# Kernel tuning notes

Measured on AMD Instinct MI355X. Metric: run time of the kernel, lower is better.

## Reference

```python
import jax, jax.numpy as jnp
import numpy as np

EMBED_DIM = 512
N_HEADS = 8
HEAD_DIM = EMBED_DIM // N_HEADS


def setup_inputs() -> dict:
    key = jax.random.key(0)
    ks = jax.random.split(key, 8)
    B, S, D = 8, 2048, EMBED_DIM
    scale = 1.0 / np.sqrt(D)
    return {
        "key": jax.random.normal(ks[0], (B, S, D), dtype=jnp.float32),
        "query": jax.random.normal(ks[1], (B, S, D), dtype=jnp.float32),
        "value": jax.random.normal(ks[2], (B, S, D), dtype=jnp.float32),
        # nn.Linear stores weight as [out, in]; y = x @ W.T. We store W_T=[in,out].
        "Wq": jax.random.normal(ks[3], (D, D), dtype=jnp.float32) * scale,
        "Wk": jax.random.normal(ks[4], (D, D), dtype=jnp.float32) * scale,
        "Wv": jax.random.normal(ks[5], (D, D), dtype=jnp.float32) * scale,
        "Wo": jax.random.normal(ks[6], (D, D), dtype=jnp.float32) * scale,
        "bo": jax.random.normal(ks[7], (D,), dtype=jnp.float32) * scale,
    }


def reference(key, query, value, Wq, Wk, Wv, Wo, bo):
    B, S, D = key.shape
    Sq = query.shape[1]
    H, Hd = N_HEADS, HEAD_DIM
    # projections (no bias for q/k/v)
    q = (query @ Wq).reshape(B, Sq, H, Hd)
    k = (key @ Wk).reshape(B, S, H, Hd)
    v = (value @ Wv).reshape(B, S, H, Hd)
    # scores: [B, H, Sq, S]
    product = jnp.einsum("bqhd,bkhd->bhqk", q, k) / np.sqrt(Hd)
    scores = jax.nn.softmax(product, axis=-1)
    out = jnp.einsum("bhqk,bkhd->bqhd", scores, v).reshape(B, Sq, D)
    return out @ Wo + bo
```

## Files before the change

### kernel.cpp

```cpp
#include <hip/hip_runtime.h>

typedef _Float16 half8 __attribute__((ext_vector_type(8)));
typedef _Float16 half4 __attribute__((ext_vector_type(4)));
typedef __fp16 fp16x2 __attribute__((ext_vector_type(2)));
typedef float floatx16 __attribute__((ext_vector_type(16)));
typedef unsigned int uint2v __attribute__((ext_vector_type(2)));

#define MFMA_F16 __builtin_amdgcn_mfma_f32_32x32x16_f16

__device__ __forceinline__ float fast_exp2(float x) {
#if __has_builtin(__builtin_amdgcn_exp2f)
    return __builtin_amdgcn_exp2f(x);
#else
    return exp2f(x);
#endif
}

__device__ __forceinline__ half4 pack4(float a, float b, float c, float d) {
    union { fp16x2 p[2]; half4 h; } u;
    u.p[0] = __builtin_amdgcn_cvt_pkrtz(a, b);
    u.p[1] = __builtin_amdgcn_cvt_pkrtz(c, d);
    return u.h;
}

__device__ __forceinline__ unsigned int pk2(float a, float b) {
    union { fp16x2 p; unsigned int u; } v;
    v.p = __builtin_amdgcn_cvt_pkrtz(a, b);
    return v.u;
}

__device__ __forceinline__ half8 ld_frag_lds(const _Float16* p) {
    union { half8 v; half4 h[2]; } u;
    u.h[0] = *(const half4*)(p);
    u.h[1] = *(const half4*)(p + 4);
    return u.v;
}

__device__ __forceinline__ half8 pv_frag(const unsigned int* w, int i0) {
    uint2v s0 = __builtin_amdgcn_permlane32_swap(w[2 * i0 + 0], w[2 * i0 + 2], false, false);
    uint2v s1 = __builtin_amdgcn_permlane32_swap(w[2 * i0 + 1], w[2 * i0 + 3], false, false);
    union { unsigned int u[4]; half8 h; } pu;
    pu.u[0] = s0[0];
    pu.u[1] = s1[0];
    pu.u[2] = s0[1];
    pu.u[3] = s1[1];
    return pu.h;
}

__global__ __launch_bounds__(256) void wcvt_kernel(const float* __restrict__ Wq,
                                                   const float* __restrict__ Wk,
                                                   const float* __restrict__ Wv,
                                                   const float* __restrict__ Wo,
                                                   _Float16* __restrict__ Wt) {
    __shared__ _Float16 T[64 * 68];
    const int bx   = blockIdx.x;
    const int wsel = bx >> 6;
    const int tile = bx & 63;
    const int to   = (tile >> 3) * 64;
    const int ti   = (tile & 7) * 64;
    const float* src = (wsel == 0) ? Wq : (wsel == 1) ? Wk : (wsel == 2) ? Wv : Wo;
    const int t = threadIdx.x;
    const int rloc = t >> 4, c4 = (t & 15) * 4;
#pragma unroll
    for (int m = 0; m < 4; m++) {
        int i = ti + rloc + 16 * m;
        float4 f = *(const float4*)(src + (size_t)i * 512 + to + c4);
        T[(c4 + 0) * 68 + rloc + 16 * m] = (_Float16)f.x;
        T[(c4 + 1) * 68 + rloc + 16 * m] = (_Float16)f.y;
        T[(c4 + 2) * 68 + rloc + 16 * m] = (_Float16)f.z;
        T[(c4 + 3) * 68 + rloc + 16 * m] = (_Float16)f.w;
    }
    __syncthreads();
    const int o_loc = t >> 2, ich = (t & 3) * 16;
    const _Float16* s = &T[o_loc * 68 + ich];
    _Float16* dst = Wt + (size_t)wsel * 262144 + (size_t)(to + o_loc) * 512 + ti + ich;
    half4 a0 = *(const half4*)(s);
    half4 a1 = *(const half4*)(s + 4);
    half4 a2 = *(const half4*)(s + 8);
    half4 a3 = *(const half4*)(s + 12);
    *(half4*)(dst)      = a0;
    *(half4*)(dst + 4)  = a1;
    *(half4*)(dst + 8)  = a2;
    *(half4*)(dst + 12) = a3;
}

__global__ __launch_bounds__(256, 3) void qkv_gemm(const float* __restrict__ query,
                                                   const float* __restrict__ key,
                                                   const float* __restrict__ value,
                                                   const _Float16* __restrict__ Wt,
                                                   _Float16* __restrict__ Qh,
                                                   _Float16* __restrict__ Kh,
                                                   _Float16* __restrict__ Vt,
                                                   float C1) {
    __shared__ _Float16 Alds[128 * 68];
    __shared__ _Float16 Blds[128 * 68];

    const int z = blockIdx.z;
    const float* A = (z == 0) ? query : (z == 1) ? key : value;
    const _Float16* W = Wt + (size_t)z * 262144;

    const int tid  = threadIdx.x;
    const int lane = tid & 63;
    const int w    = tid >> 6;
    const int l31  = lane & 31;
    const int lh   = lane >> 5;
    const int wm   = w >> 1;
    const int wn   = w & 1;
    const int n0   = blockIdx.x * 128;
    const int m0   = blockIdx.y * 128;
    const int crow = tid >> 3;
    const int ck8  = (tid & 7) * 8;

    floatx16 acc[2][2];
#pragma unroll
    for (int i = 0; i < 2; i++)
#pragma unroll
        for (int j = 0; j < 2; j++)
#pragma unroll
            for (int r = 0; r < 16; r++) acc[i][j][r] = 0.0f;

    float4 apre[4][2];
    int4   bpre[4];
#pragma unroll
    for (int i = 0; i < 4; i++) {
        const float* p = A + (size_t)(m0 + crow + 32 * i) * 512 + ck8;
        apre[i][0] = *(const float4*)(p);
        apre[i][1] = *(const float4*)(p + 4);
        bpre[i] = *(const int4*)(W + (size_t)(n0 + crow + 32 * i) * 512 + ck8);
    }

    for (int t = 0; t < 8; t++) {
        __syncthreads();
#pragma unroll
        for (int i = 0; i < 4; i++) {
            int r = crow + 32 * i;
            float4 f0 = apre[i][0], f1 = apre[i][1];
            *(half4*)&Alds[r * 68 + ck8]     = pack4(f0.x, f0.y, f0.z, f0.w);
            *(half4*)&Alds[r * 68 + ck8 + 4] = pack4(f1.x, f1.y, f1.z, f1.w);
            *(int2*)&Blds[r * 68 + ck8]      = make_int2(bpre[i].x, bpre[i].y);
            *(int2*)&Blds[r * 68 + ck8 + 4]  = make_int2(bpre[i].z, bpre[i].w);
        }
        __syncthreads();
        if (t < 7) {
            int ks2 = (t + 1) * 64;
#pragma unroll
            for (int i = 0; i < 4; i++) {
                const float* p = A + (size_t)(m0 + crow + 32 * i) * 512 + ks2 + ck8;
                apre[i][0] = *(const float4*)(p);
                apre[i][1] = *(const float4*)(p + 4);
                bpre[i] = *(const int4*)(W + (size_t)(n0 + crow + 32 * i) * 512 + ks2 + ck8);
            }
        }
#pragma unroll
        for (int kc = 0; kc < 4; kc++) {
            int kb = kc * 16 + lh * 8;
            half8 af[2], bf[2];
            af[0] = ld_frag_lds(&Alds[(wm * 64 + l31) * 68 + kb]);
            af[1] = ld_frag_lds(&Alds[(wm * 64 + 32 + l31) * 68 + kb]);
            bf[0] = ld_frag_lds(&Blds[(wn * 64 + l31) * 68 + kb]);
            bf[1] = ld_frag_lds(&Blds[(wn * 64 + 32 + l31) * 68 + kb]);
#pragma unroll
            for (int i = 0; i < 2; i++)
#pragma unroll
                for (int j = 0; j < 2; j++)
                    acc[i][j] = MFMA_F16(af[i], bf[j], acc[i][j], 0, 0, 0);
        }
    }

    const float oscale = (z == 0) ? C1 : 1.0f;
    _Float16* out01 = (z == 0) ? Qh : Kh;
#pragma unroll
    for (int i = 0; i < 2; i++) {
#pragma unroll
        for (int j = 0; j < 2; j++) {
            int gn    = n0 + wn * 64 + j * 32 + l31;
            int mbase = m0 + wm * 64 + i * 32 + 4 * lh;
            int h = gn >> 6, hd = gn & 63;
            if (z < 2) {
#pragma unroll
                for (int r = 0; r < 16; r++) {
                    int gm = mbase + (r & 3) + 8 * (r >> 2);
                    int b = gm >> 11, s = gm & 2047;
                    out01[(size_t)((b * 8 + h) * 2048 + s) * 64 + hd] =
                        (_Float16)(acc[i][j][r] * oscale);
                }
            } else {
#pragma unroll
                for (int g = 0; g < 4; g++) {
                    int gm = mbase + 8 * g;
                    int b = gm >> 11, s = gm & 2047;
                    *(half4*)&Vt[(size_t)((b * 8 + h) * 64 + hd) * 2048 + s] =
                        pack4(acc[i][j][4 * g + 0], acc[i][j][4 * g + 1],
                              acc[i][j][4 * g + 2], acc[i][j][4 * g + 3]);
                }
            }
        }
    }
}

__global__ __launch_bounds__(256, 3) void out_gemm(const _Float16* __restrict__ A,
                                                   const _Float16* __restrict__ W,
                                                   const float* __restrict__ bias,
                                                   float* __restrict__ out) {
    __shared__ _Float16 Alds[128 * 68];
    __shared__ _Float16 Blds[128 * 68];

    const int tid  = threadIdx.x;
    const int lane = tid & 63;
    const int w    = tid >> 6;
    const int l31  = lane & 31;
    const int lh   = lane >> 5;
    const int wm   = w >> 1;
    const int wn   = w & 1;
    const int n0   = blockIdx.x * 128;
    const int m0   = blockIdx.y * 128;
    const int crow = tid >> 3;
    const int ck8  = (tid & 7) * 8;

    floatx16 acc[2][2];
#pragma unroll
    for (int i = 0; i < 2; i++)
#pragma unroll
        for (int j = 0; j < 2; j++)
#pragma unroll
            for (int r = 0; r < 16; r++) acc[i][j][r] = 0.0f;

    int4 apre[4], bpre[4];
#pragma unroll
    for (int i = 0; i < 4; i++) {
        apre[i] = *(const int4*)(A + (size_t)(m0 + crow + 32 * i) * 512 + ck8);
        bpre[i] = *(const int4*)(W + (size_t)(n0 + crow + 32 * i) * 512 + ck8);
    }

    for (int t = 0; t < 8; t++) {
        __syncthreads();
#pragma unroll
        for (int i = 0; i < 4; i++) {
            int r = crow + 32 * i;
            *(int2*)&Alds[r * 68 + ck8]     = make_int2(apre[i].x, apre[i].y);
            *(int2*)&Alds[r * 68 + ck8 + 4] = make_int2(apre[i].z, apre[i].w);
            *(int2*)&Blds[r * 68 + ck8]     = make_int2(bpre[i].x, bpre[i].y);
            *(int2*)&Blds[r * 68 + ck8 + 4] = make_int2(bpre[i].z, bpre[i].w);
        }
        __syncthreads();
        if (t < 7) {
            int ks2 = (t + 1) * 64;
#pragma unroll
            for (int i = 0; i < 4; i++) {
                apre[i] = *(const int4*)(A + (size_t)(m0 + crow + 32 * i) * 512 + ks2 + ck8);
                bpre[i] = *(const int4*)(W + (size_t)(n0 + crow + 32 * i) * 512 + ks2 + ck8);
            }
        }
#pragma unroll
        for (int kc = 0; kc < 4; kc++) {
            int kb = kc * 16 + lh * 8;
            half8 af[2], bf[2];
            af[0] = ld_frag_lds(&Alds[(wm * 64 + l31) * 68 + kb]);
            af[1] = ld_frag_lds(&Alds[(wm * 64 + 32 + l31) * 68 + kb]);
            bf[0] = ld_frag_lds(&Blds[(wn * 64 + l31) * 68 + kb]);
            bf[1] = ld_frag_lds(&Blds[(wn * 64 + 32 + l31) * 68 + kb]);
#pragma unroll
            for (int i = 0; i < 2; i++)
#pragma unroll
                for (int j = 0; j < 2; j++)
                    acc[i][j] = MFMA_F16(af[i], bf[j], acc[i][j], 0, 0, 0);
        }
    }

#pragma unroll
    for (int i = 0; i < 2; i++) {
#pragma unroll
        for (int j = 0; j < 2; j++) {
            int gn    = n0 + wn * 64 + j * 32 + l31;
            int mbase = m0 + wm * 64 + i * 32 + 4 * lh;
            float bv = bias[gn];
#pragma unroll
            for (int r = 0; r < 16; r++) {
                int gm = mbase + (r & 3) + 8 * (r >> 2);
                out[(size_t)gm * 512 + gn] = acc[i][j][r] + bv;
            }
        }
    }
}

__global__ __launch_bounds__(256, 3) void attn_kernel(const _Float16* __restrict__ Qg,
                                                      const _Float16* __restrict__ Kg,
                                                      const _Float16* __restrict__ Vg,
                                                      _Float16* __restrict__ AO) {
    __shared__ _Float16 Kbuf[2][64 * 68];
    __shared__ _Float16 Vbuf[2][64 * 68];

    const int tid  = threadIdx.x;
    const int lane = tid & 63;
    const int w    = tid >> 6;
    const int l31  = lane & 31;
    const int lh   = lane >> 5;
    const int h    = blockIdx.y;
    const int b    = blockIdx.z;
    const int q0   = blockIdx.x * 128 + w * 32;

    const size_t bhoff = (size_t)(b * 8 + h) * (2048 * 64);
    const _Float16* Qbh = Qg + bhoff;
    const _Float16* Kbh = Kg + bhoff;
    const _Float16* Vbh = Vg + bhoff;

    const int c0row = tid >> 3, ck8 = (tid & 7) * 8;
    const int c1row = c0row + 32;

    half8 qf[4];
#pragma unroll
    for (int kc = 0; kc < 4; kc++)
        qf[kc] = *(const half8*)(Qbh + (size_t)(q0 + l31) * 64 + kc * 16 + lh * 8);

    floatx16 O[2];
#pragma unroll
    for (int i = 0; i < 2; i++)
#pragma unroll
        for (int r = 0; r < 16; r++) O[i][r] = 0.0f;
    float lsum = 0.0f;

    unsigned int w16[16];
    half8 vf[4][2];

    int4 kpre[2], vpre[2];
    kpre[0] = *(const int4*)(Kbh + c0row * 64 + ck8);
    kpre[1] = *(const int4*)(Kbh + c1row * 64 + ck8);
    vpre[0] = *(const int4*)(Vbh + (size_t)c0row * 2048 + ck8);
    vpre[1] = *(const int4*)(Vbh + (size_t)c1row * 2048 + ck8);
    *(int2*)&Kbuf[0][c0row * 68 + ck8]     = make_int2(kpre[0].x, kpre[0].y);
    *(int2*)&Kbuf[0][c0row * 68 + ck8 + 4] = make_int2(kpre[0].z, kpre[0].w);
    *(int2*)&Kbuf[0][c1row * 68 + ck8]     = make_int2(kpre[1].x, kpre[1].y);
    *(int2*)&Kbuf[0][c1row * 68 + ck8 + 4] = make_int2(kpre[1].z, kpre[1].w);
    *(int2*)&Vbuf[0][c0row * 68 + ck8]     = make_int2(vpre[0].x, vpre[0].y);
    *(int2*)&Vbuf[0][c0row * 68 + ck8 + 4] = make_int2(vpre[0].z, vpre[0].w);
    *(int2*)&Vbuf[0][c1row * 68 + ck8]     = make_int2(vpre[1].x, vpre[1].y);
    *(int2*)&Vbuf[0][c1row * 68 + ck8 + 4] = make_int2(vpre[1].z, vpre[1].w);
    kpre[0] = *(const int4*)(Kbh + 4096 + c0row * 64 + ck8);
    kpre[1] = *(const int4*)(Kbh + 4096 + c1row * 64 + ck8);
    vpre[0] = *(const int4*)(Vbh + 64 + (size_t)c0row * 2048 + ck8);
    vpre[1] = *(const int4*)(Vbh + 64 + (size_t)c1row * 2048 + ck8);
    __syncthreads();

    for (int kt = 0; kt < 32; kt++) {
        const int cur = kt & 1;
        const _Float16* Kc = Kbuf[cur];
        const _Float16* Vc = Vbuf[cur];

        if (kt > 0) {
#pragma unroll
            for (int kc = 0; kc < 4; kc++) {
                int i0 = (kc >> 1) * 4 + (kc & 1) * 2;
                half8 pf = pv_frag(w16, i0);
                O[0] = MFMA_F16(vf[kc][0], pf, O[0], 0, 0, 0);
                O[1] = MFMA_F16(vf[kc][1], pf, O[1], 0, 0, 0);
            }
        }

        if (kt < 31) {
            _Float16* Kd = Kbuf[cur ^ 1];
            _Float16* Vd = Vbuf[cur ^ 1];
            *(int2*)&Kd[c0row * 68 + ck8]     = make_int2(kpre[0].x, kpre[0].y);
            *(int2*)&Kd[c0row * 68 + ck8 + 4] = make_int2(kpre[0].z, kpre[0].w);
            *(int2*)&Kd[c1row * 68 + ck8]     = make_int2(kpre[1].x, kpre[1].y);
            *(int2*)&Kd[c1row * 68 + ck8 + 4] = make_int2(kpre[1].z, kpre[1].w);
            *(int2*)&Vd[c0row * 68 + ck8]     = make_int2(vpre[0].x, vpre[0].y);
            *(int2*)&Vd[c0row * 68 + ck8 + 4] = make_int2(vpre[0].z, vpre[0].w);
            *(int2*)&Vd[c1row * 68 + ck8]     = make_int2(vpre[1].x, vpre[1].y);
            *(int2*)&Vd[c1row * 68 + ck8 + 4] = make_int2(vpre[1].z, vpre[1].w);
        }
        if (kt < 30) {
            const _Float16* Ksrc = Kbh + (size_t)(kt + 2) * 4096;
            const _Float16* Vsrc = Vbh + (size_t)(kt + 2) * 64;
            kpre[0] = *(const int4*)(Ksrc + c0row * 64 + ck8);
            kpre[1] = *(const int4*)(Ksrc + c1row * 64 + ck8);
            vpre[0] = *(const int4*)(Vsrc + (size_t)c0row * 2048 + ck8);
            vpre[1] = *(const int4*)(Vsrc + (size_t)c1row * 2048 + ck8);
        }

#pragma unroll
        for (int kc = 0; kc < 4; kc++) {
            vf[kc][0] = ld_frag_lds(&Vc[(l31)*68      + kc * 16 + lh * 8]);
            vf[kc][1] = ld_frag_lds(&Vc[(32 + l31)*68 + kc * 16 + lh * 8]);
        }

        floatx16 Sf[2];
#pragma unroll
        for (int i = 0; i < 2; i++)
#pragma unroll
            for (int r = 0; r < 16; r++) Sf[i][r] = 0.0f;
#pragma unroll
        for (int kc = 0; kc < 4; kc++) {
#pragma unroll
            for (int ms = 0; ms < 2; ms++) {
                half8 kf = ld_frag_lds(&Kc[(ms * 32 + l31) * 68 + kc * 16 + lh * 8]);
                Sf[ms] = MFMA_F16(kf, qf[kc], Sf[ms], 0, 0, 0);
            }
        }

        float rsA = 0.0f, rsB = 0.0f;
#pragma unroll
        for (int i = 0; i < 8; i++) {
            int ms = i >> 2, g = i & 3;
            float p0 = fast_exp2(Sf[ms][4 * g + 0]);
            float p1 = fast_exp2(Sf[ms][4 * g + 1]);
            float p2 = fast_exp2(Sf[ms][4 * g + 2]);
            float p3 = fast_exp2(Sf[ms][4 * g + 3]);
            rsA += p0 + p1;
            rsB += p2 + p3;
            w16[2 * i + 0] = pk2(p0, p1);
            w16[2 * i + 1] = pk2(p2, p3);
        }
        lsum += rsA + rsB;

        __syncthreads();
    }

#pragma unroll
    for (int kc = 0; kc < 4; kc++) {
        int i0 = (kc >> 1) * 4 + (kc & 1) * 2;
        half8 pf = pv_frag(w16, i0);
        O[0] = MFMA_F16(vf[kc][0], pf, O[0], 0, 0, 0);
        O[1] = MFMA_F16(vf[kc][1], pf, O[1], 0, 0, 0);
    }

    lsum += __shfl_xor(lsum, 32);
    float inv = 1.0f / lsum;
    int q = q0 + l31;
#pragma unroll
    for (int hs = 0; hs < 2; hs++) {
#pragma unroll
        for (int g = 0; g < 4; g++) {
            *(half4*)&AO[(size_t)(b * 2048 + q) * 512 + h * 64 + hs * 32 + g * 8 + lh * 4] =
                pack4(O[hs][4 * g + 0] * inv, O[hs][4 * g + 1] * inv,
                      O[hs][4 * g + 2] * inv, O[hs][4 * g + 3] * inv);
        }
    }
}

extern "C" void kernel_launch(void* const* d_in, const int* in_sizes, int n_in,
                              void* d_out, int out_size, void* d_ws, size_t ws_size,
                              hipStream_t stream) {
    const float* key   = (const float*)d_in[0];
    const float* query = (const float*)d_in[1];
    const float* value = (const float*)d_in[2];
    const float* Wq    = (const float*)d_in[3];
    const float* Wk    = (const float*)d_in[4];
    const float* Wv    = (const float*)d_in[5];
    const float* Wo    = (const float*)d_in[6];
    const float* bo    = (const float*)d_in[7];

    _Float16* ws = (_Float16*)d_ws;
    _Float16* Wt = ws;
    _Float16* Qh = ws + 1048576;
    _Float16* Kh = Qh + 8388608;
    _Float16* Vt = Kh + 8388608;
    _Float16* AO = Vt + 8388608;

    const float C1 = 0.18033688011112042f;

    wcvt_kernel<<<dim3(256), dim3(256), 0, stream>>>(Wq, Wk, Wv, Wo, Wt);

    qkv_gemm<<<dim3(4, 128, 3), dim3(256), 0, stream>>>(query, key, value, Wt,
                                                        Qh, Kh, Vt, C1);

    attn_kernel<<<dim3(16, 8, 8), dim3(256), 0, stream>>>(Qh, Kh, Vt, AO);

    out_gemm<<<dim3(4, 128), dim3(256), 0, stream>>>(AO, Wt + 3 * 262144, bo,
                                                     (float*)d_out);
}
```

Measured before the change: 290.2 us.

## Process 64 query rows per wave in attention to reuse K/V tiles

```diff
diff --git a/kernel.cpp b/kernel.cpp
--- a/kernel.cpp
+++ b/kernel.cpp
@@ -283,7 +283,7 @@
     }
 }
 
-__global__ __launch_bounds__(256, 3) void attn_kernel(const _Float16* __restrict__ Qg,
+__global__ __launch_bounds__(256, 2) void attn_kernel(const _Float16* __restrict__ Qg,
                                                       const _Float16* __restrict__ Kg,
                                                       const _Float16* __restrict__ Vg,
                                                       _Float16* __restrict__ AO) {
@@ -297,7 +297,7 @@
     const int lh   = lane >> 5;
     const int h    = blockIdx.y;
     const int b    = blockIdx.z;
-    const int q0   = blockIdx.x * 128 + w * 32;
+    const int q0   = blockIdx.x * 256 + w * 64;
 
     const size_t bhoff = (size_t)(b * 8 + h) * (2048 * 64);
     const _Float16* Qbh = Qg + bhoff;
@@ -307,19 +307,24 @@
     const int c0row = tid >> 3, ck8 = (tid & 7) * 8;
     const int c1row = c0row + 32;
 
-    half8 qf[4];
+    half8 qf[4][2];
 #pragma unroll
     for (int kc = 0; kc < 4; kc++)
-        qf[kc] = *(const half8*)(Qbh + (size_t)(q0 + l31) * 64 + kc * 16 + lh * 8);
-
-    floatx16 O[2];
+#pragma unroll
+        for (int qs = 0; qs < 2; qs++)
+            qf[kc][qs] = *(const half8*)(Qbh + (size_t)(q0 + qs * 32 + l31) * 64 +
+                                         kc * 16 + lh * 8);
+
+    floatx16 O[2][2];
 #pragma unroll
     for (int i = 0; i < 2; i++)
 #pragma unroll
-        for (int r = 0; r < 16; r++) O[i][r] = 0.0f;
-    float lsum = 0.0f;
-
-    unsigned int w16[16];
+        for (int j = 0; j < 2; j++)
+#pragma unroll
+            for (int r = 0; r < 16; r++) O[i][j][r] = 0.0f;
+    float lsum0 = 0.0f, lsum1 = 0.0f;
+
+    unsigned int w16[2][16];
     half8 vf[4][2];
 
     int4 kpre[2], vpre[2];
@@ -347,13 +352,18 @@
         const _Float16* Vc = Vbuf[cur];
 
         if (kt > 0) {
+            __builtin_amdgcn_s_setprio(1);
 #pragma unroll
             for (int kc = 0; kc < 4; kc++) {
                 int i0 = (kc >> 1) * 4 + (kc & 1) * 2;
-                half8 pf = pv_frag(w16, i0);
-                O[0] = MFMA_F16(vf[kc][0], pf, O[0], 0, 0, 0);
-                O[1] = MFMA_F16(vf[kc][1], pf, O[1], 0, 0, 0);
-            }
+                half8 pf0 = pv_frag(w16[0], i0);
+                half8 pf1 = pv_frag(w16[1], i0);
+                O[0][0] = MFMA_F16(vf[kc][0], pf0, O[0][0], 0, 0, 0);
+                O[1][0] = MFMA_F16(vf[kc][1], pf0, O[1][0], 0, 0, 0);
+                O[0][1] = MFMA_F16(vf[kc][0], pf1, O[0][1], 0, 0, 0);
+                O[1][1] = MFMA_F16(vf[kc][1], pf1, O[1][1], 0, 0, 0);
+            }
+            __builtin_amdgcn_s_setprio(0);
         }
 
         if (kt < 31) {
@@ -383,56 +393,88 @@
             vf[kc][1] = ld_frag_lds(&Vc[(32 + l31)*68 + kc * 16 + lh * 8]);
         }
 
-        floatx16 Sf[2];
+        floatx16 Sf[2][2];
 #pragma unroll
         for (int i = 0; i < 2; i++)
 #pragma unroll
-            for (int r = 0; r < 16; r++) Sf[i][r] = 0.0f;
+            for (int j = 0; j < 2; j++)
+#pragma unroll
+                for (int r = 0; r < 16; r++) Sf[i][j][r] = 0.0f;
 #pragma unroll
         for (int kc = 0; kc < 4; kc++) {
 #pragma unroll
             for (int ms = 0; ms < 2; ms++) {
                 half8 kf = ld_frag_lds(&Kc[(ms * 32 + l31) * 68 + kc * 16 + lh * 8]);
-                Sf[ms] = MFMA_F16(kf, qf[kc], Sf[ms], 0, 0, 0);
-            }
-        }
-
-        float rsA = 0.0f, rsB = 0.0f;
-#pragma unroll
-        for (int i = 0; i < 8; i++) {
-            int ms = i >> 2, g = i & 3;
-            float p0 = fast_exp2(Sf[ms][4 * g + 0]);
-            float p1 = fast_exp2(Sf[ms][4 * g + 1]);
-            float p2 = fast_exp2(Sf[ms][4 * g + 2]);
-            float p3 = fast_exp2(Sf[ms][4 * g + 3]);
-            rsA += p0 + p1;
-            rsB += p2 + p3;
-            w16[2 * i + 0] = pk2(p0, p1);
-            w16[2 * i + 1] = pk2(p2, p3);
-        }
-        lsum += rsA + rsB;
+                Sf[ms][0] = MFMA_F16(kf, qf[kc][0], Sf[ms][0], 0, 0, 0);
+                Sf[ms][1] = MFMA_F16(kf, qf[kc][1], Sf[ms][1], 0, 0, 0);
+            }
+        }
+
+        {
+            float rsA = 0.0f, rsB = 0.0f;
+#pragma unroll
+            for (int i = 0; i < 8; i++) {
+                int ms = i >> 2, g = i & 3;
+                float p0 = fast_exp2(Sf[ms][0][4 * g + 0]);
+                float p1 = fast_exp2(Sf[ms][0][4 * g + 1]);
+                float p2 = fast_exp2(Sf[ms][0][4 * g + 2]);
+                float p3 = fast_exp2(Sf[ms][0][4 * g + 3]);
+                rsA += p0 + p1;
+                rsB += p2 + p3;
+                w16[0][2 * i + 0] = pk2(p0, p1);
+                w16[0][2 * i + 1] = pk2(p2, p3);
+            }
+            lsum0 += rsA + rsB;
+        }
+        {
+            float rsA = 0.0f, rsB = 0.0f;
+#pragma unroll
+            for (int i = 0; i < 8; i++) {
+                int ms = i >> 2, g = i & 3;
+                float p0 = fast_exp2(Sf[ms][1][4 * g + 0]);
+                float p1 = fast_exp2(Sf[ms][1][4 * g + 1]);
+                float p2 = fast_exp2(Sf[ms][1][4 * g + 2]);
+                float p3 = fast_exp2(Sf[ms][1][4 * g + 3]);
+                rsA += p0 + p1;
+                rsB += p2 + p3;
+                w16[1][2 * i + 0] = pk2(p0, p1);
+                w16[1][2 * i + 1] = pk2(p2, p3);
+            }
+            lsum1 += rsA + rsB;
+        }
 
         __syncthreads();
     }
 
+    __builtin_amdgcn_s_setprio(1);
 #pragma unroll
     for (int kc = 0; kc < 4; kc++) {
         int i0 = (kc >> 1) * 4 + (kc & 1) * 2;
-        half8 pf = pv_frag(w16, i0);
-        O[0] = MFMA_F16(vf[kc][0], pf, O[0], 0, 0, 0);
-        O[1] = MFMA_F16(vf[kc][1], pf, O[1], 0, 0, 0);
-    }
-
-    lsum += __shfl_xor(lsum, 32);
-    float inv = 1.0f / lsum;
-    int q = q0 + l31;
-#pragma unroll
-    for (int hs = 0; hs < 2; hs++) {
-#pragma unroll
-        for (int g = 0; g < 4; g++) {
-            *(half4*)&AO[(size_t)(b * 2048 + q) * 512 + h * 64 + hs * 32 + g * 8 + lh * 4] =
-                pack4(O[hs][4 * g + 0] * inv, O[hs][4 * g + 1] * inv,
-                      O[hs][4 * g + 2] * inv, O[hs][4 * g + 3] * inv);
+        half8 pf0 = pv_frag(w16[0], i0);
+        half8 pf1 = pv_frag(w16[1], i0);
+        O[0][0] = MFMA_F16(vf[kc][0], pf0, O[0][0], 0, 0, 0);
+        O[1][0] = MFMA_F16(vf[kc][1], pf0, O[1][0], 0, 0, 0);
+        O[0][1] = MFMA_F16(vf[kc][0], pf1, O[0][1], 0, 0, 0);
+        O[1][1] = MFMA_F16(vf[kc][1], pf1, O[1][1], 0, 0, 0);
+    }
+    __builtin_amdgcn_s_setprio(0);
+
+    lsum0 += __shfl_xor(lsum0, 32);
+    lsum1 += __shfl_xor(lsum1, 32);
+    float inv0 = 1.0f / lsum0;
+    float inv1 = 1.0f / lsum1;
+#pragma unroll
+    for (int qs = 0; qs < 2; qs++) {
+        float inv = (qs == 0) ? inv0 : inv1;
+        int q = q0 + qs * 32 + l31;
+#pragma unroll
+        for (int hs = 0; hs < 2; hs++) {
+#pragma unroll
+            for (int g = 0; g < 4; g++) {
+                *(half4*)&AO[(size_t)(b * 2048 + q) * 512 + h * 64 + hs * 32 + g * 8 + lh * 4] =
+                    pack4(O[hs][qs][4 * g + 0] * inv, O[hs][qs][4 * g + 1] * inv,
+                          O[hs][qs][4 * g + 2] * inv, O[hs][qs][4 * g + 3] * inv);
+            }
         }
     }
 }
@@ -463,7 +505,7 @@
     qkv_gemm<<<dim3(4, 128, 3), dim3(256), 0, stream>>>(query, key, value, Wt,
                                                         Qh, Kh, Vt, C1);
 
-    attn_kernel<<<dim3(16, 8, 8), dim3(256), 0, stream>>>(Qh, Kh, Vt, AO);
+    attn_kernel<<<dim3(8, 8, 8), dim3(256), 0, stream>>>(Qh, Kh, Vt, AO);
 
     out_gemm<<<dim3(4, 128), dim3(256), 0, stream>>>(AO, Wt + 3 * 262144, bo,
                                                      (float*)d_out);
```

Measured after the change: 379.1 us. 30.6% more time.

## Load V fragments directly from global memory, dropping V LDS staging

Applied to the files above, without the earlier changes.

```diff
diff --git a/kernel.cpp b/kernel.cpp
--- a/kernel.cpp
+++ b/kernel.cpp
@@ -34,6 +34,12 @@
     u.h[0] = *(const half4*)(p);
     u.h[1] = *(const half4*)(p + 4);
     return u.v;
+}
+
+__device__ __forceinline__ void tile_barrier() {
+    asm volatile("s_waitcnt lgkmcnt(0)" ::: "memory");
+    __builtin_amdgcn_s_barrier();
+    asm volatile("" ::: "memory");
 }
 
 __device__ __forceinline__ half8 pv_frag(const unsigned int* w, int i0) {
@@ -288,7 +294,6 @@
                                                       const _Float16* __restrict__ Vg,
                                                       _Float16* __restrict__ AO) {
     __shared__ _Float16 Kbuf[2][64 * 68];
-    __shared__ _Float16 Vbuf[2][64 * 68];
 
     const int tid  = threadIdx.x;
     const int lane = tid & 63;
@@ -304,6 +309,9 @@
     const _Float16* Kbh = Kg + bhoff;
     const _Float16* Vbh = Vg + bhoff;
 
+    const _Float16* Vrow0 = Vbh + (size_t)l31 * 2048 + lh * 8;
+    const _Float16* Vrow1 = Vbh + (size_t)(32 + l31) * 2048 + lh * 8;
+
     const int c0row = tid >> 3, ck8 = (tid & 7) * 8;
     const int c1row = c0row + 32;
 
@@ -320,107 +328,93 @@
     float lsum = 0.0f;
 
     unsigned int w16[16];
-    half8 vf[4][2];
-
-    int4 kpre[2], vpre[2];
+    half8 vfA[4][2], vfB[4][2];
+
+    int4 kpre[2];
     kpre[0] = *(const int4*)(Kbh + c0row * 64 + ck8);
     kpre[1] = *(const int4*)(Kbh + c1row * 64 + ck8);
-    vpre[0] = *(const int4*)(Vbh + (size_t)c0row * 2048 + ck8);
-    vpre[1] = *(const int4*)(Vbh + (size_t)c1row * 2048 + ck8);
     *(int2*)&Kbuf[0][c0row * 68 + ck8]     = make_int2(kpre[0].x, kpre[0].y);
     *(int2*)&Kbuf[0][c0row * 68 + ck8 + 4] = make_int2(kpre[0].z, kpre[0].w);
     *(int2*)&Kbuf[0][c1row * 68 + ck8]     = make_int2(kpre[1].x, kpre[1].y);
     *(int2*)&Kbuf[0][c1row * 68 + ck8 + 4] = make_int2(kpre[1].z, kpre[1].w);
-    *(int2*)&Vbuf[0][c0row * 68 + ck8]     = make_int2(vpre[0].x, vpre[0].y);
-    *(int2*)&Vbuf[0][c0row * 68 + ck8 + 4] = make_int2(vpre[0].z, vpre[0].w);
-    *(int2*)&Vbuf[0][c1row * 68 + ck8]     = make_int2(vpre[1].x, vpre[1].y);
-    *(int2*)&Vbuf[0][c1row * 68 + ck8 + 4] = make_int2(vpre[1].z, vpre[1].w);
     kpre[0] = *(const int4*)(Kbh + 4096 + c0row * 64 + ck8);
     kpre[1] = *(const int4*)(Kbh + 4096 + c1row * 64 + ck8);
-    vpre[0] = *(const int4*)(Vbh + 64 + (size_t)c0row * 2048 + ck8);
-    vpre[1] = *(const int4*)(Vbh + 64 + (size_t)c1row * 2048 + ck8);
-    __syncthreads();
-
-    for (int kt = 0; kt < 32; kt++) {
-        const int cur = kt & 1;
-        const _Float16* Kc = Kbuf[cur];
-        const _Float16* Vc = Vbuf[cur];
-
-        if (kt > 0) {
-#pragma unroll
-            for (int kc = 0; kc < 4; kc++) {
-                int i0 = (kc >> 1) * 4 + (kc & 1) * 2;
-                half8 pf = pv_frag(w16, i0);
-                O[0] = MFMA_F16(vf[kc][0], pf, O[0], 0, 0, 0);
-                O[1] = MFMA_F16(vf[kc][1], pf, O[1], 0, 0, 0);
-            }
-        }
-
-        if (kt < 31) {
-            _Float16* Kd = Kbuf[cur ^ 1];
-            _Float16* Vd = Vbuf[cur ^ 1];
-            *(int2*)&Kd[c0row * 68 + ck8]     = make_int2(kpre[0].x, kpre[0].y);
-            *(int2*)&Kd[c0row * 68 + ck8 + 4] = make_int2(kpre[0].z, kpre[0].w);
-            *(int2*)&Kd[c1row * 68 + ck8]     = make_int2(kpre[1].x, kpre[1].y);
-            *(int2*)&Kd[c1row * 68 + ck8 + 4] = make_int2(kpre[1].z, kpre[1].w);
-            *(int2*)&Vd[c0row * 68 + ck8]     = make_int2(vpre[0].x, vpre[0].y);
-            *(int2*)&Vd[c0row * 68 + ck8 + 4] = make_int2(vpre[0].z, vpre[0].w);
-            *(int2*)&Vd[c1row * 68 + ck8]     = make_int2(vpre[1].x, vpre[1].y);
-            *(int2*)&Vd[c1row * 68 + ck8 + 4] = make_int2(vpre[1].z, vpre[1].w);
-        }
-        if (kt < 30) {
-            const _Float16* Ksrc = Kbh + (size_t)(kt + 2) * 4096;
-            const _Float16* Vsrc = Vbh + (size_t)(kt + 2) * 64;
-            kpre[0] = *(const int4*)(Ksrc + c0row * 64 + ck8);
-            kpre[1] = *(const int4*)(Ksrc + c1row * 64 + ck8);
-            vpre[0] = *(const int4*)(Vsrc + (size_t)c0row * 2048 + ck8);
-            vpre[1] = *(const int4*)(Vsrc + (size_t)c1row * 2048 + ck8);
-        }
-
-#pragma unroll
-        for (int kc = 0; kc < 4; kc++) {
-            vf[kc][0] = ld_frag_lds(&Vc[(l31)*68      + kc * 16 + lh * 8]);
-            vf[kc][1] = ld_frag_lds(&Vc[(32 + l31)*68 + kc * 16 + lh * 8]);
-        }
-
-        floatx16 Sf[2];
-#pragma unroll
-        for (int i = 0; i < 2; i++)
-#pragma unroll
-            for (int r = 0; r < 16; r++) Sf[i][r] = 0.0f;
-#pragma unroll
-        for (int kc = 0; kc < 4; kc++) {
-#pragma unroll
-            for (int ms = 0; ms < 2; ms++) {
-                half8 kf = ld_frag_lds(&Kc[(ms * 32 + l31) * 68 + kc * 16 + lh * 8]);
-                Sf[ms] = MFMA_F16(kf, qf[kc], Sf[ms], 0, 0, 0);
-            }
-        }
-
-        float rsA = 0.0f, rsB = 0.0f;
-#pragma unroll
-        for (int i = 0; i < 8; i++) {
-            int ms = i >> 2, g = i & 3;
-            float p0 = fast_exp2(Sf[ms][4 * g + 0]);
-            float p1 = fast_exp2(Sf[ms][4 * g + 1]);
-            float p2 = fast_exp2(Sf[ms][4 * g + 2]);
-            float p3 = fast_exp2(Sf[ms][4 * g + 3]);
-            rsA += p0 + p1;
-            rsB += p2 + p3;
-            w16[2 * i + 0] = pk2(p0, p1);
-            w16[2 * i + 1] = pk2(p2, p3);
-        }
-        lsum += rsA + rsB;
-
-        __syncthreads();
-    }
+    tile_barrier();
+
+#define ATTN_ITER(KT, VFU, VFF, KCUR, KNXT, DO_D, DO_F, DO_G)                 \
+    {                                                                          \
+             \
+        _Pragma("unroll")                                                      \
+        for (int kc = 0; kc < 4; kc++) {                                       \
+            VFF[kc][0] = *(const half8*)(Vrow0 + (KT) * 64 + kc * 16);         \
+            VFF[kc][1] = *(const half8*)(Vrow1 + (KT) * 64 + kc * 16);         \
+        }                                                                      \
+        if (DO_D) {                                                            \
+                       \
+            _Pragma("unroll")                                                  \
+            for (int kc = 0; kc < 4; kc++) {                                   \
+                int i0 = (kc >> 1) * 4 + (kc & 1) * 2;                         \
+                half8 pf = pv_frag(w16, i0);                                   \
+                O[0] = MFMA_F16(VFU[kc][0], pf, O[0], 0, 0, 0);                \
+                O[1] = MFMA_F16(VFU[kc][1], pf, O[1], 0, 0, 0);                \
+            }                                                                  \
+        }                                                                      \
+        if (DO_F) {                 \
+            _Float16* Kd = (KNXT);                                             \
+            *(int2*)&Kd[c0row * 68 + ck8]     = make_int2(kpre[0].x, kpre[0].y); \
+            *(int2*)&Kd[c0row * 68 + ck8 + 4] = make_int2(kpre[0].z, kpre[0].w); \
+            *(int2*)&Kd[c1row * 68 + ck8]     = make_int2(kpre[1].x, kpre[1].y); \
+            *(int2*)&Kd[c1row * 68 + ck8 + 4] = make_int2(kpre[1].z, kpre[1].w); \
+        }                                                                      \
+        if (DO_G) {                                    \
+            const _Float16* Ksrc = Kbh + (size_t)((KT) + 2) * 4096;            \
+            kpre[0] = *(const int4*)(Ksrc + c0row * 64 + ck8);                 \
+            kpre[1] = *(const int4*)(Ksrc + c1row * 64 + ck8);                 \
+        }                                                                      \
+                                                      \
+        floatx16 Sf[2];                                                        \
+        _Pragma("unroll")                                                      \
+        for (int i = 0; i < 2; i++)                                            \
+            _Pragma("unroll")                                                  \
+            for (int r = 0; r < 16; r++) Sf[i][r] = 0.0f;                      \
+        _Pragma("unroll")                                                      \
+        for (int kc = 0; kc < 4; kc++) {                                       \
+            _Pragma("unroll")                                                  \
+            for (int ms = 0; ms < 2; ms++) {                                   \
+                half8 kf = ld_frag_lds(&(KCUR)[(ms * 32 + l31) * 68 + kc * 16 + lh * 8]); \
+                Sf[ms] = MFMA_F16(kf, qf[kc], Sf[ms], 0, 0, 0);                \
+            }                                                                  \
+        }                                                                      \
+                   \
+        float rsA = 0.0f, rsB = 0.0f;                                          \
+        _Pragma("unroll")                                                      \
+        for (int i = 0; i < 8; i++) {                                          \
+            int ms = i >> 2, g = i & 3;                                        \
+            float p0 = fast_exp2(Sf[ms][4 * g + 0]);                           \
+            float p1 = fast_exp2(Sf[ms][4 * g + 1]);                           \
+            float p2 = fast_exp2(Sf[ms][4 * g + 2]);                           \
+            float p3 = fast_exp2(Sf[ms][4 * g + 3]);                           \
+            rsA += p0 + p1;                                                    \
+            rsB += p2 + p3;                                                    \
+            w16[2 * i + 0] = pk2(p0, p1);                                      \
+            w16[2 * i + 1] = pk2(p2, p3);                                      \
+        }                                                                      \
+        lsum += rsA + rsB;                                                     \
+        tile_barrier();                                                        \
+    }
+
+    for (int kt2 = 0; kt2 < 32; kt2 += 2) {
+        ATTN_ITER(kt2,     vfB, vfA, Kbuf[0], Kbuf[1], (kt2 > 0), true,       (kt2 < 30));
+        ATTN_ITER(kt2 + 1, vfA, vfB, Kbuf[1], Kbuf[0], true,      (kt2 < 30), (kt2 + 1 < 30));
+    }
+#undef ATTN_ITER
 
 #pragma unroll
     for (int kc = 0; kc < 4; kc++) {
         int i0 = (kc >> 1) * 4 + (kc & 1) * 2;
         half8 pf = pv_frag(w16, i0);
-        O[0] = MFMA_F16(vf[kc][0], pf, O[0], 0, 0, 0);
-        O[1] = MFMA_F16(vf[kc][1], pf, O[1], 0, 0, 0);
+        O[0] = MFMA_F16(vfB[kc][0], pf, O[0], 0, 0, 0);
+        O[1] = MFMA_F16(vfB[kc][1], pf, O[1], 0, 0, 0);
     }
 
     lsum += __shfl_xor(lsum, 32);
```

New measurement: 357.5 us. 1.23x slower.
